# Performance work log

Measured on AMD Instinct MI355X. Metric: run time of the kernel, lower is better.

The kernel has to match this reference:

```python
import jax, jax.numpy as jnp
import numpy as np

N, E, H, OUT, L = 50000, 500000, 256, 128, 2
EPS = 1e-5  # torch LayerNorm default


def _make_edges(k):
    # both rows cover all N nodes so that unique()/remap in the original is identity
    k1, k2, kp = jax.random.split(k, 3)
    row0 = jnp.concatenate([jax.random.permutation(kp, N), jax.random.randint(k1, (E - N,), 0, N)])
    row1 = jnp.concatenate([jnp.arange(N), jax.random.randint(k2, (E - N,), 0, N)])
    return jnp.stack([row0, row1]).astype(jnp.int32)


def setup_inputs() -> dict:
    key = jax.random.key(0)
    ks = jax.random.split(key, 7)
    s = 0.02
    x = jax.random.normal(ks[0], (N, H), jnp.float32)
    edge_r1 = _make_edges(ks[1])
    edge_r2 = _make_edges(ks[2])
    Wl = jax.random.normal(ks[3], (L, H, H), jnp.float32) * s
    W0 = jax.random.normal(ks[4], (L, H, H), jnp.float32) * s
    W1 = jax.random.normal(ks[5], (L, H, H), jnp.float32) * s
    bl = jnp.zeros((L, H), jnp.float32)
    b0 = jnp.zeros((L, H), jnp.float32)
    b1 = jnp.zeros((L, H), jnp.float32)
    gamma = jnp.ones((L, H), jnp.float32)
    beta = jnp.zeros((L, H), jnp.float32)
    Wout = jax.random.normal(ks[6], (OUT, H), jnp.float32) * s
    bout = jnp.zeros((OUT,), jnp.float32)
    return dict(x=x, edge_r1=edge_r1, edge_r2=edge_r2, Wl=Wl, bl=bl, W0=W0, b0=b0,
                W1=W1, b1=b1, gamma=gamma, beta=beta, Wout=Wout, bout=bout)


def _layer(i, h, x0, e, Wl, bl, W0, b0, W1, b1, gamma, beta):
    # PyG flow='target_to_source', aggr='add': gather h at e[1], scatter-add at e[0]
    agg = jax.ops.segment_sum(h[e[1]], e[0], num_segments=h.shape[0])  # [N, H]
    z = agg @ Wl[i].T + bl[i] + h @ W0[i].T + b0[i] + x0 @ W1[i].T + b1[i]
    z = jax.nn.relu(z)
    mu = jnp.mean(z, axis=-1, keepdims=True)
    var = jnp.mean(jnp.square(z - mu), axis=-1, keepdims=True)
    return (z - mu) * jax.lax.rsqrt(var + EPS) * gamma[i] + beta[i]  # dropout is identity in eval


def reference(x, edge_r1, edge_r2, Wl, bl, W0, b0, W1, b1, gamma, beta, Wout, bout):
    # reversed(metapath): (C,r2,C) with conv_idx=1 first, then (C,r1,C) with conv_idx=0
    h = _layer(1, x, x, edge_r2, Wl, bl, W0, b0, W1, b1, gamma, beta)
    h = _layer(0, h, x, edge_r1, Wl, bl, W0, b0, W1, b1, gamma, beta)
    return h @ Wout.T + bout  # [N, OUT]
```

## Files before the change

kernel.cpp:

```cpp
#include <hip/hip_runtime.h>
#include <stdint.h>

#define N_NODES 50000
#define N_EDGES 500000
#define NPAD    50048
#define NBLK    128
#define EPB     4096
#define NBUCK   391
#define LFLAT   50048
#define NSC2    196
#define P4CAP   4096
#define EPS     1e-5f

typedef _Float16 half8_ __attribute__((ext_vector_type(8)));
typedef _Float16 half4_ __attribute__((ext_vector_type(4)));
typedef float    float4_ __attribute__((ext_vector_type(4)));

typedef uint32_t u32_g __attribute__((address_space(1)));
typedef uint32_t u32_s __attribute__((address_space(3)));

__device__ __forceinline__ void gload16(const void* g, void* lds_wave_base) {
    __builtin_amdgcn_global_load_lds((const u32_g*)g, (u32_s*)lds_wave_base, 16, 0, 0);
}

__global__ __launch_bounds__(256) void prep_kernel(
        const int* __restrict__ e1, const int* __restrict__ e2,
        int* __restrict__ G, unsigned short* __restrict__ rank16,
        const float* __restrict__ x, _Float16* __restrict__ xh,
        _Float16* __restrict__ aggb, _Float16* __restrict__ h1,
        const float* __restrict__ Wl, const float* __restrict__ W0,
        const float* __restrict__ W1, const float* __restrict__ Wout,
        _Float16* __restrict__ Wcat,
        const float* __restrict__ bl, const float* __restrict__ b0,
        const float* __restrict__ b1, const float* __restrict__ bout,
        float* __restrict__ bias,
        unsigned long long* __restrict__ states) {
    __shared__ int hist[NBUCK];
    const int bid = blockIdx.x;
    const int tid = threadIdx.x;
    if (bid < 256) {
        const int s = bid >> 7, blk = bid & 127;
        const int* dst = s ? e2 : e1;
        unsigned short* rk = rank16 + (size_t)s * N_EDGES;
        for (int b = tid; b < NBUCK; b += 256) hist[b] = 0;
        __syncthreads();
        const int e0 = blk * EPB;
        int myrank[16];
#pragma unroll
        for (int k = 0; k < 16; k++) {
            int i = e0 + k * 256 + tid;
            int r = 0;
            if (i < N_EDGES) r = atomicAdd(&hist[dst[i] >> 7], 1);
            myrank[k] = r;
        }
#pragma unroll
        for (int k = 0; k < 16; k++) {
            int i = e0 + k * 256 + tid;
            if (i < N_EDGES) rk[i] = (unsigned short)myrank[k];
        }
        __syncthreads();
        int* Gp = G + (s * NBLK + blk) * NBUCK;
        for (int b = tid; b < NBUCK; b += 256) Gp[b] = hist[b];
    } else if (bid < 12756) {
        int i = (bid - 256) * 256 + tid;
        float4_ v = ((const float4_*)x)[i];
        half4_ h;
        h[0] = (_Float16)v[0]; h[1] = (_Float16)v[1];
        h[2] = (_Float16)v[2]; h[3] = (_Float16)v[3];
        ((half4_*)xh)[i] = h;
    } else if (bid < 14420) {
        int i = (bid - 12756) * 256 + tid;
        if (i < 2 * 256 * 768) {
            int l = i / (256 * 768);
            int r = i % (256 * 768);
            int j = r / 768, k = r % 768;
            const float* s = (k < 256) ? Wl : (k < 512 ? W0 : W1);
            Wcat[i] = (_Float16)s[l * 65536 + j * 256 + (k & 255)];
        } else {
            Wcat[i] = (_Float16)Wout[i - 2 * 256 * 768];
        }
    } else if (bid < 14456) {
        int j = (bid - 14420) * 256 + tid;
        int buf = j / 3072, jj = j % 3072;
        _Float16* p = (buf == 0) ? xh : (buf == 1) ? aggb : h1;
        half4_ z = {(_Float16)0.f, (_Float16)0.f, (_Float16)0.f, (_Float16)0.f};
        *(half4_*)(p + (size_t)N_NODES * 256 + (size_t)jj * 4) = z;
    } else if (bid < 14459) {
        int i = (bid - 14456) * 256 + tid;
        if (i < 512)      bias[i] = bl[i] + b0[i] + b1[i];
        else if (i < 640) bias[i] = bout[i - 512];
    } else {
        for (int i = tid; i < 2 * NSC2; i += 256) states[i] = 0ULL;
    }
}

__global__ __launch_bounds__(256) void p2_scan(const int* __restrict__ G,
                                               unsigned long long* __restrict__ state,
                                               int* __restrict__ start2) {
    __shared__ int sm[256];
    __shared__ int s_excl;
    const int bid = blockIdx.x;
    const int s = bid / NSC2;
    const int seq = bid % NSC2;
    const int t = threadIdx.x;
    const int i = seq * 256 + t;
    unsigned long long* st = state + s * NSC2;

    int v = 0;
    if (i < LFLAT) v = G[(s * NBLK + (i & 127)) * NBUCK + (i >> 7)];
    sm[t] = v;
    __syncthreads();
    for (int off = 1; off < 256; off <<= 1) {
        int x = sm[t];
        if (t >= off) x += sm[t - off];
        __syncthreads();
        sm[t] = x;
        __syncthreads();
    }
    int total = sm[255];

    if (t == 0) {
        if (seq == 0) {
            atomicExch(&st[0], (2ULL << 32) | (unsigned int)total);
            s_excl = 0;
        } else {
            atomicExch(&st[seq], (1ULL << 32) | (unsigned int)total);
            int running = 0;
            int j = seq - 1;
            while (true) {
                unsigned long long sv = atomicAdd(&st[j], 0ULL);
                unsigned int tag = (unsigned int)(sv >> 32);
                if (tag == 0) continue;
                running += (int)(unsigned int)sv;
                if (tag == 2) break;
                j--;
            }
            atomicExch(&st[seq], (2ULL << 32) | (unsigned int)(running + total));
            s_excl = running;
        }
    }
    __syncthreads();
    if (i < LFLAT) start2[s * LFLAT + i] = s_excl + sm[t] - v;
}

__global__ __launch_bounds__(256) void p3_scatter(const int* __restrict__ e1,
                                                  const int* __restrict__ e2,
                                                  const unsigned short* __restrict__ rank16,
                                                  const int* __restrict__ start2,
                                                  unsigned int* __restrict__ tmp) {
    const int bid = blockIdx.x;
    const int s = bid >> 7, blk = bid & 127;
    const int t = threadIdx.x;
    const int* ed = s ? e2 : e1;
    const int* st = start2 + s * LFLAT;
    const unsigned short* rk = rank16 + (size_t)s * N_EDGES;
    unsigned int* tp = tmp + (size_t)s * N_EDGES;
    const int e0 = blk * EPB;
#pragma unroll
    for (int k = 0; k < 16; k++) {
        int i = e0 + k * 256 + t;
        if (i < N_EDGES) {
            int d   = ed[i];
            int src = ed[N_EDGES + i];
            int pos = st[(d >> 7) * NBLK + blk] + (int)rk[i];
            tp[pos] = ((unsigned)(d & 127) << 16) | (unsigned)src;
        }
    }
}

__global__ __launch_bounds__(256) void p4_build(const unsigned int* __restrict__ tmp,
                                                const int* __restrict__ start2,
                                                int* __restrict__ rp,
                                                int* __restrict__ col) {
    __shared__ int cnt[128];
    __shared__ int off[128];
    __shared__ unsigned int   stM[P4CAP];
    __shared__ unsigned short stS[P4CAP];
    const int b = blockIdx.x;
    const int s = blockIdx.y;
    const int t = threadIdx.x;
    const int* st = start2 + s * LFLAT;
    const int A   = st[b * NBLK];
    const int Bnd = (b == NBUCK - 1) ? N_EDGES : st[(b + 1) * NBLK];
    const unsigned int* tp = tmp + (size_t)s * N_EDGES;

    if (t < 128) cnt[t] = 0;
    __syncthreads();
    for (int eb = A; eb < Bnd; eb += 256) {
        int e = eb + t;
        if (e < Bnd) {
            unsigned v = tp[e];
            int idx = (int)(v >> 16);
            int r = atomicAdd(&cnt[idx], 1);
            int sl = e - A;
            if (sl < P4CAP) {
                stM[sl] = ((unsigned)idx << 12) | (unsigned)r;
                stS[sl] = (unsigned short)(v & 0xFFFFu);
            }
        }
    }
    __syncthreads();
    if (t < 128) off[t] = cnt[t];
    __syncthreads();
    for (int d = 1; d < 128; d <<= 1) {
        int x = 0;
        if (t < 128) { x = off[t]; if (t >= d) x += off[t - d]; }
        __syncthreads();
        if (t < 128) off[t] = x;
        __syncthreads();
    }
    const int nE = Bnd - A;
    int* colS = col + (size_t)s * N_EDGES;
    for (int sl = t; sl < nE && sl < P4CAP; sl += 256) {
        unsigned m = stM[sl];
        int idx = (int)(m >> 12), r = (int)(m & 4095u);
        colS[A + off[idx] - cnt[idx] + r] = (int)stS[sl];
    }
    const int nbase = b * 128;
    if (t < 128 && nbase + t < N_NODES)
        rp[s * (N_NODES + 1) + nbase + t] = A + off[t] - cnt[t];
    if (b == NBUCK - 1 && t == 0) rp[s * (N_NODES + 1) + N_NODES] = N_EDGES;
}

__global__ void gather_kernel(const _Float16* __restrict__ hin,
                              const int* __restrict__ rowptr, const int* __restrict__ col,
                              _Float16* __restrict__ dst, int n) {
    int node = blockIdx.x * 4 + (threadIdx.x >> 6);
    int lane = threadIdx.x & 63;
    int half = lane >> 5, l5 = lane & 31;
    if (node >= n) return;
    int s = rowptr[node], e = rowptr[node + 1];
    float a[8] = {0.f, 0.f, 0.f, 0.f, 0.f, 0.f, 0.f, 0.f};
    float b[8] = {0.f, 0.f, 0.f, 0.f, 0.f, 0.f, 0.f, 0.f};
    int i = s + half;
    for (; i + 6 < e; i += 8) {
        int c0 = col[i], c1 = col[i + 2], c2 = col[i + 4], c3 = col[i + 6];
        half8_ v0 = *(const half8_*)(hin + (size_t)c0 * 256 + l5 * 8);
        half8_ v1 = *(const half8_*)(hin + (size_t)c1 * 256 + l5 * 8);
        half8_ v2 = *(const half8_*)(hin + (size_t)c2 * 256 + l5 * 8);
        half8_ v3 = *(const half8_*)(hin + (size_t)c3 * 256 + l5 * 8);
#pragma unroll
        for (int j = 0; j < 8; j++) {
            a[j] += (float)v0[j] + (float)v2[j];
            b[j] += (float)v1[j] + (float)v3[j];
        }
    }
    for (; i < e; i += 2) {
        int c0 = col[i];
        half8_ v0 = *(const half8_*)(hin + (size_t)c0 * 256 + l5 * 8);
#pragma unroll
        for (int j = 0; j < 8; j++) a[j] += (float)v0[j];
    }
    half8_ o;
#pragma unroll
    for (int j = 0; j < 8; j++) {
        float t = a[j] + b[j];
        t += __shfl_xor(t, 32, 64);
        o[j] = (_Float16)t;
    }
    if (half == 0)
        *(half8_*)(dst + (size_t)node * 256 + l5 * 8) = o;
}

__global__ __launch_bounds__(512) void gemm_ln(const _Float16* __restrict__ agg,
                                               const _Float16* __restrict__ hsrc,
                                               const _Float16* __restrict__ xh,
                                               const _Float16* __restrict__ Bw,
                                               const float* __restrict__ bias,
                                               const float* __restrict__ gamma,
                                               const float* __restrict__ beta,
                                               _Float16* __restrict__ H,
                                               const _Float16* __restrict__ Wfin,
                                               const float* __restrict__ bfin,
                                               float* __restrict__ outp) {
    __shared__ __align__(16) char smem[49152];
    char* AsB = smem;
    char* BsB = smem + 16384;
    const int rowBase = blockIdx.x * 128;
    const int tid  = threadIdx.x;
    const int lane = tid & 63;
    const int w    = tid >> 6;
    const int wm = w & 1, wn = w >> 1;
    const int quad = lane >> 4, mr = lane & 15;
    const int x7 = mr & 7;

    float4_ acc[4][4];
#pragma unroll
    for (int i = 0; i < 4; i++)
#pragma unroll
        for (int j = 0; j < 4; j++) { float4_ z4 = {0.f, 0.f, 0.f, 0.f}; acc[i][j] = z4; }

    int cA0 = w * 64 + lane, cA1 = cA0 + 512;
    int rA0 = cA0 >> 3, rA1 = cA1 >> 3;
    size_t offA0 = (size_t)(rowBase + rA0) * 256 + (((cA0 & 7) ^ (rA0 & 7)) * 8);
    size_t offA1 = (size_t)(rowBase + rA1) * 256 + (((cA1 & 7) ^ (rA1 & 7)) * 8);
    size_t offB[4];
#pragma unroll
    for (int j = 0; j < 4; j++) {
        int c = j * 512 + w * 64 + lane;
        int r = c >> 3;
        offB[j] = (size_t)r * 768 + (((c & 7) ^ (r & 7)) * 8);
    }
    void* lA0 = AsB + w * 1024;
    void* lA1 = AsB + 8192 + w * 1024;

    for (int k0 = 0; k0 < 768; k0 += 64) {
        const _Float16* src = (k0 < 256) ? agg : (k0 < 512) ? hsrc : xh;
        const int kloc = k0 & 255;
        gload16(src + offA0 + kloc, lA0);
        gload16(src + offA1 + kloc, lA1);
        gload16(Bw + offB[0] + k0, BsB + w * 1024);
        gload16(Bw + offB[1] + k0, BsB + 8192 + w * 1024);
        gload16(Bw + offB[2] + k0, BsB + 16384 + w * 1024);
        gload16(Bw + offB[3] + k0, BsB + 24576 + w * 1024);
        __syncthreads();
#pragma unroll
        for (int s = 0; s < 2; s++) {
            half8_ a[4], b[4];
#pragma unroll
            for (int im = 0; im < 4; im++) {
                int row = wm * 64 + im * 16 + mr;
                a[im] = *(const half8_*)(AsB + row * 128 + (((s * 4 + quad) ^ x7) * 16));
            }
#pragma unroll
            for (int in = 0; in < 4; in++) {
                int row = wn * 64 + in * 16 + mr;
                b[in] = *(const half8_*)(BsB + row * 128 + (((s * 4 + quad) ^ x7) * 16));
            }
#pragma unroll
            for (int im = 0; im < 4; im++)
#pragma unroll
                for (int in = 0; in < 4; in++)
                    acc[im][in] = __builtin_amdgcn_mfma_f32_16x16x32_f16(a[im], b[in], acc[im][in], 0, 0, 0);
        }
        __syncthreads();
    }

    float bv[4], gv[4], bev[4];
#pragma unroll
    for (int in = 0; in < 4; in++) {
        int colg = wn * 64 + in * 16 + mr;
        bv[in]  = bias[colg];
        gv[in]  = gamma[colg];
        bev[in] = beta[colg];
    }
    float* lnbuf   = (float*)AsB;
    float* lnstats = (float*)(AsB + 4096);

#pragma unroll
    for (int im = 0; im < 4; im++)
#pragma unroll
        for (int r = 0; r < 4; r++) {
            float s = 0.f, sq = 0.f;
#pragma unroll
            for (int in = 0; in < 4; in++) {
                float v = acc[im][in][r] + bv[in];
                v = v > 0.f ? v : 0.f;
                s += v; sq += v * v;
            }
            s  += __shfl_xor(s, 1, 64);  sq += __shfl_xor(sq, 1, 64);
            s  += __shfl_xor(s, 2, 64);  sq += __shfl_xor(sq, 2, 64);
            s  += __shfl_xor(s, 4, 64);  sq += __shfl_xor(sq, 4, 64);
            s  += __shfl_xor(s, 8, 64);  sq += __shfl_xor(sq, 8, 64);
            if (mr == 0) {
                int rl = wm * 64 + im * 16 + quad * 4 + r;
                lnbuf[(wn * 128 + rl) * 2]     = s;
                lnbuf[(wn * 128 + rl) * 2 + 1] = sq;
            }
        }
    __syncthreads();
    if (tid < 128) {
        float s  = lnbuf[tid * 2]             + lnbuf[(128 + tid) * 2]
                 + lnbuf[(256 + tid) * 2]     + lnbuf[(384 + tid) * 2];
        float sq = lnbuf[tid * 2 + 1]         + lnbuf[(128 + tid) * 2 + 1]
                 + lnbuf[(256 + tid) * 2 + 1] + lnbuf[(384 + tid) * 2 + 1];
        float mu  = s * (1.0f / 256.0f);
        float var = sq * (1.0f / 256.0f) - mu * mu;
        lnstats[tid * 2]     = mu;
        lnstats[tid * 2 + 1] = rsqrtf(var + EPS);
    }
    __syncthreads();

    _Float16* BsH = (_Float16*)BsB;
#pragma unroll
    for (int p = 0; p < 2; p++) {
        if (wm == p) {
#pragma unroll
            for (int im = 0; im < 4; im++)
#pragma unroll
                for (int r = 0; r < 4; r++) {
                    int rl = im * 16 + quad * 4 + r;
                    float mu = lnstats[(p * 64 + rl) * 2];
                    float rs = lnstats[(p * 64 + rl) * 2 + 1];
#pragma unroll
                    for (int in = 0; in < 4; in++) {
                        float v = acc[im][in][r] + bv[in];
                        v = v > 0.f ? v : 0.f;
                        BsH[rl * 256 + wn * 64 + in * 16 + mr] =
                            (_Float16)((v - mu) * rs * gv[in] + bev[in]);
                    }
                }
        }
        __syncthreads();
#pragma unroll
        for (int i = 0; i < 4; i++) {
            int c = i * 512 + tid;
            int row = c >> 5, ch = c & 31;
            half8_ v = *(const half8_*)(BsB + c * 16);
            *(half8_*)(H + (size_t)(rowBase + p * 64 + row) * 256 + ch * 8) = v;
        }
        __syncthreads();
    }

    if (Wfin != nullptr) {
        const int wm2 = w & 1;
        const int wn2 = w >> 1;
        float4_ oacc[4][2];
#pragma unroll
        for (int ir = 0; ir < 4; ir++)
#pragma unroll
            for (int ic = 0; ic < 2; ic++) { float4_ z4 = {0.f, 0.f, 0.f, 0.f}; oacc[ir][ic] = z4; }
        const _Float16* hG = H + (size_t)(rowBase + w * 16 + (lane >> 2)) * 256 + (lane & 3) * 8;
        void* lA = AsB + w * 1024;
#pragma unroll
        for (int k0 = 0; k0 < 256; k0 += 32) {
            gload16(hG + k0, lA);
            __syncthreads();
            half8_ a2[4], b2[2];
#pragma unroll
            for (int ir = 0; ir < 4; ir++)
                a2[ir] = *(const half8_*)(AsB + (wm2 * 64 + ir * 16 + mr) * 64 + quad * 16);
#pragma unroll
            for (int ic = 0; ic < 2; ic++)
                b2[ic] = *(const half8_*)(Wfin + (size_t)(wn2 * 32 + ic * 16 + mr) * 256 + k0 + quad * 8);
#pragma unroll
            for (int ir = 0; ir < 4; ir++)
#pragma unroll
                for (int ic = 0; ic < 2; ic++)
                    oacc[ir][ic] = __builtin_amdgcn_mfma_f32_16x16x32_f16(a2[ir], b2[ic], oacc[ir][ic], 0, 0, 0);
            __syncthreads();
        }
#pragma unroll
        for (int ic = 0; ic < 2; ic++) {
            int colg = wn2 * 32 + ic * 16 + mr;
            float bb = bfin[colg];
#pragma unroll
            for (int ir = 0; ir < 4; ir++) {
#pragma unroll
                for (int r = 0; r < 4; r++) {
                    int row = rowBase + wm2 * 64 + ir * 16 + quad * 4 + r;
                    if (row < N_NODES) outp[(size_t)row * 128 + colg] = oacc[ir][ic][r] + bb;
                }
            }
        }
    }
}

extern "C" void kernel_launch(void* const* d_in, const int* in_sizes, int n_in,
                              void* d_out, int out_size, void* d_ws, size_t ws_size,
                              hipStream_t stream) {
    const float* x    = (const float*)d_in[0];
    const int*   e1   = (const int*)d_in[1];
    const int*   e2   = (const int*)d_in[2];
    const float* Wl   = (const float*)d_in[3];
    const float* bl   = (const float*)d_in[4];
    const float* W0   = (const float*)d_in[5];
    const float* b0   = (const float*)d_in[6];
    const float* W1   = (const float*)d_in[7];
    const float* b1   = (const float*)d_in[8];
    const float* gamma= (const float*)d_in[9];
    const float* beta = (const float*)d_in[10];
    const float* Wout = (const float*)d_in[11];
    const float* bout = (const float*)d_in[12];

    char* ws = (char*)d_ws;
    size_t off = 0;
    auto alloc = [&](size_t bytes) -> char* {
        char* p = ws + off;
        off = (off + bytes + 255) & ~(size_t)255;
        return p;
    };
    _Float16* xh   = (_Float16*)alloc((size_t)NPAD * 256 * 2);
    _Float16* aggb = (_Float16*)alloc((size_t)NPAD * 256 * 2);
    _Float16* h1   = (_Float16*)alloc((size_t)NPAD * 256 * 2);
    _Float16* h2   = (_Float16*)alloc((size_t)NPAD * 256 * 2);
    _Float16* Wcat = (_Float16*)alloc((size_t)(2 * 256 * 768 + 128 * 256) * 2);
    float*    bias = (float*)alloc(640 * 4);
    unsigned long long* states = (unsigned long long*)alloc((size_t)2 * NSC2 * 8);
    int* G      = (int*)alloc((size_t)2 * NBLK * NBUCK * 4);
    int* start2 = (int*)alloc((size_t)2 * LFLAT * 4);
    int* rp     = (int*)alloc((size_t)2 * (N_NODES + 1) * 4);
    unsigned short* rank16 = (unsigned short*)alloc((size_t)2 * N_EDGES * 2);
    unsigned int*   tmp    = (unsigned int*)alloc((size_t)2 * N_EDGES * 4);
    int* col    = (int*)alloc((size_t)2 * N_EDGES * 4);

    int* rp1 = rp, *rp2 = rp + (N_NODES + 1);
    int* col1 = col, *col2 = col + N_EDGES;

    prep_kernel<<<14460, 256, 0, stream>>>(e1, e2, G, rank16, x, xh, aggb, h1,
                                           Wl, W0, W1, Wout, Wcat,
                                           bl, b0, b1, bout, bias, states);
    p2_scan<<<2 * NSC2, 256, 0, stream>>>(G, states, start2);
    p3_scatter<<<256, 256, 0, stream>>>(e1, e2, rank16, start2, tmp);
    p4_build<<<dim3(NBUCK, 2), 256, 0, stream>>>(tmp, start2, rp, col);

    const int nb4 = (N_NODES + 3) / 4;
    const _Float16* WoutH = Wcat + 393216;

    gather_kernel<<<nb4, 256, 0, stream>>>(xh, rp2, col2, aggb, N_NODES);
    gemm_ln<<<391, 512, 0, stream>>>(aggb, xh, xh, Wcat + 196608,
                                     bias + 256, gamma + 256, beta + 256, h1,
                                     nullptr, nullptr, nullptr);
    gather_kernel<<<nb4, 256, 0, stream>>>(h1, rp1, col1, aggb, N_NODES);
    gemm_ln<<<391, 512, 0, stream>>>(aggb, h1, xh, Wcat,
                                     bias, gamma, beta, h2,
                                     WoutH, bias + 512, (float*)d_out);
}
```

Baseline: 319.1 us.

## Fuse neighbor aggregation gather into the GEMM+LayerNorm kernel prologue

Removes the separate gather kernel and has each gemm_ln block compute the aggregated neighbor sums for its own 128 rows before the GEMM, writing them to global memory and syncing. This saves two kernel launches and lets each block reuse its freshly written rows from cache. In exchange the gather runs with far fewer, serially-iterating waves (each half-wave walks 8 nodes in sequence), which reduces memory-level parallelism for the random row loads.

```diff
diff --git a/kernel.cpp b/kernel.cpp
--- a/kernel.cpp
+++ b/kernel.cpp
@@ -222,49 +222,11 @@
     if (b == NBUCK - 1 && t == 0) rp[s * (N_NODES + 1) + N_NODES] = N_EDGES;
 }
 
-__global__ void gather_kernel(const _Float16* __restrict__ hin,
-                              const int* __restrict__ rowptr, const int* __restrict__ col,
-                              _Float16* __restrict__ dst, int n) {
-    int node = blockIdx.x * 4 + (threadIdx.x >> 6);
-    int lane = threadIdx.x & 63;
-    int half = lane >> 5, l5 = lane & 31;
-    if (node >= n) return;
-    int s = rowptr[node], e = rowptr[node + 1];
-    float a[8] = {0.f, 0.f, 0.f, 0.f, 0.f, 0.f, 0.f, 0.f};
-    float b[8] = {0.f, 0.f, 0.f, 0.f, 0.f, 0.f, 0.f, 0.f};
-    int i = s + half;
-    for (; i + 6 < e; i += 8) {
-        int c0 = col[i], c1 = col[i + 2], c2 = col[i + 4], c3 = col[i + 6];
-        half8_ v0 = *(const half8_*)(hin + (size_t)c0 * 256 + l5 * 8);
-        half8_ v1 = *(const half8_*)(hin + (size_t)c1 * 256 + l5 * 8);
-        half8_ v2 = *(const half8_*)(hin + (size_t)c2 * 256 + l5 * 8);
-        half8_ v3 = *(const half8_*)(hin + (size_t)c3 * 256 + l5 * 8);
-#pragma unroll
-        for (int j = 0; j < 8; j++) {
-            a[j] += (float)v0[j] + (float)v2[j];
-            b[j] += (float)v1[j] + (float)v3[j];
-        }
-    }
-    for (; i < e; i += 2) {
-        int c0 = col[i];
-        half8_ v0 = *(const half8_*)(hin + (size_t)c0 * 256 + l5 * 8);
-#pragma unroll
-        for (int j = 0; j < 8; j++) a[j] += (float)v0[j];
-    }
-    half8_ o;
-#pragma unroll
-    for (int j = 0; j < 8; j++) {
-        float t = a[j] + b[j];
-        t += __shfl_xor(t, 32, 64);
-        o[j] = (_Float16)t;
-    }
-    if (half == 0)
-        *(half8_*)(dst + (size_t)node * 256 + l5 * 8) = o;
-}
-
-__global__ __launch_bounds__(512) void gemm_ln(const _Float16* __restrict__ agg,
+__global__ __launch_bounds__(512) void gemm_ln(_Float16* __restrict__ aggb,
                                                const _Float16* __restrict__ hsrc,
                                                const _Float16* __restrict__ xh,
+                                               const int* __restrict__ rowptr,
+                                               const int* __restrict__ colx,
                                                const _Float16* __restrict__ Bw,
                                                const float* __restrict__ bias,
                                                const float* __restrict__ gamma,
@@ -284,6 +246,44 @@
     const int quad = lane >> 4, mr = lane & 15;
     const int x7 = mr & 7;
 
+    {
+        const int l5 = lane & 31;
+        const int nbase = rowBase + w * 16 + (lane >> 5) * 8;
+#pragma unroll 1
+        for (int nn = 0; nn < 8; nn++) {
+            int nd = nbase + nn;
+            if (nd < N_NODES) {
+                int s0 = rowptr[nd], e0 = rowptr[nd + 1];
+                float a[8] = {0.f, 0.f, 0.f, 0.f, 0.f, 0.f, 0.f, 0.f};
+                float b[8] = {0.f, 0.f, 0.f, 0.f, 0.f, 0.f, 0.f, 0.f};
+                int i = s0;
+                for (; i + 3 < e0; i += 4) {
+                    int c0 = colx[i], c1 = colx[i + 1], c2 = colx[i + 2], c3 = colx[i + 3];
+                    half8_ v0 = *(const half8_*)(hsrc + (size_t)c0 * 256 + l5 * 8);
+                    half8_ v1 = *(const half8_*)(hsrc + (size_t)c1 * 256 + l5 * 8);
+                    half8_ v2 = *(const half8_*)(hsrc + (size_t)c2 * 256 + l5 * 8);
+                    half8_ v3 = *(const half8_*)(hsrc + (size_t)c3 * 256 + l5 * 8);
+#pragma unroll
+                    for (int j = 0; j < 8; j++) {
+                        a[j] += (float)v0[j] + (float)v2[j];
+                        b[j] += (float)v1[j] + (float)v3[j];
+                    }
+                }
+                for (; i < e0; i++) {
+                    int c0 = colx[i];
+                    half8_ v0 = *(const half8_*)(hsrc + (size_t)c0 * 256 + l5 * 8);
+#pragma unroll
+                    for (int j = 0; j < 8; j++) a[j] += (float)v0[j];
+                }
+                half8_ o;
+#pragma unroll
+                for (int j = 0; j < 8; j++) o[j] = (_Float16)(a[j] + b[j]);
+                *(half8_*)(aggb + (size_t)nd * 256 + l5 * 8) = o;
+            }
+        }
+    }
+    __syncthreads();
+
     float4_ acc[4][4];
 #pragma unroll
     for (int i = 0; i < 4; i++)
@@ -305,7 +305,7 @@
     void* lA1 = AsB + 8192 + w * 1024;
 
     for (int k0 = 0; k0 < 768; k0 += 64) {
-        const _Float16* src = (k0 < 256) ? agg : (k0 < 512) ? hsrc : xh;
+        const _Float16* src = (k0 < 256) ? aggb : (k0 < 512) ? hsrc : xh;
         const int kloc = k0 & 255;
         gload16(src + offA0 + kloc, lA0);
         gload16(src + offA1 + kloc, lA1);
@@ -504,15 +504,12 @@
     p3_scatter<<<256, 256, 0, stream>>>(e1, e2, rank16, start2, tmp);
     p4_build<<<dim3(NBUCK, 2), 256, 0, stream>>>(tmp, start2, rp, col);
 
-    const int nb4 = (N_NODES + 3) / 4;
     const _Float16* WoutH = Wcat + 393216;
 
-    gather_kernel<<<nb4, 256, 0, stream>>>(xh, rp2, col2, aggb, N_NODES);
-    gemm_ln<<<391, 512, 0, stream>>>(aggb, xh, xh, Wcat + 196608,
+    gemm_ln<<<391, 512, 0, stream>>>(aggb, xh, xh, rp2, col2, Wcat + 196608,
                                      bias + 256, gamma + 256, beta + 256, h1,
                                      nullptr, nullptr, nullptr);
-    gather_kernel<<<nb4, 256, 0, stream>>>(h1, rp1, col1, aggb, N_NODES);
-    gemm_ln<<<391, 512, 0, stream>>>(aggb, h1, xh, Wcat,
+    gemm_ln<<<391, 512, 0, stream>>>(aggb, h1, xh, rp1, col1, Wcat,
                                      bias, gamma, beta, h2,
                                      WoutH, bias + 512, (float*)d_out);
 }
```

Result: slower. 407.7 us (+27.7%).
